# Performance work log

Hardware: AMD Instinct MI355X
Metric: run time of the kernel (lower is better)

Reference implementation:

```python
import jax, jax.numpy as jnp
import numpy as np
import math

B, S, H, NH = 2, 2048, 1024, 16
DK = H // NH


def setup_inputs() -> dict:
    key = jax.random.key(0)
    ks = jax.random.split(key, 12)
    s = 1.0 / math.sqrt(H)
    return {
        "query": jax.random.normal(ks[0], (B, S, H), jnp.float32),
        "key": jax.random.normal(ks[1], (B, S, H), jnp.float32),
        "value": jax.random.normal(ks[2], (B, S, H), jnp.float32),
        "attention_mask": jax.random.randint(ks[3], (B, S), 0, 2, jnp.int32),
        "Wq": jax.random.normal(ks[4], (H, H), jnp.float32) * s,
        "bq": jnp.zeros((H,), jnp.float32),
        "Wk": jax.random.normal(ks[5], (H, H), jnp.float32) * s,
        "bk": jnp.zeros((H,), jnp.float32),
        "Wv": jax.random.normal(ks[6], (H, H), jnp.float32) * s,
        "bv": jnp.zeros((H,), jnp.float32),
        "Wo": jax.random.normal(ks[7], (H, H), jnp.float32) * s,
        "bo": jnp.zeros((H,), jnp.float32),
    }


def reference(query, key, value, attention_mask, Wq, bq, Wk, bk, Wv, bv, Wo, bo):
    # linear projections (torch Linear: x @ W^T + b)
    q = query @ Wq.T + bq
    k = key @ Wk.T + bk
    v = value @ Wv.T + bv
    # [B, S, H] -> [B, NH, S, DK]
    q = q.reshape(B, S, NH, DK).transpose(0, 2, 1, 3)
    k = k.reshape(B, S, NH, DK).transpose(0, 2, 1, 3)
    v = v.reshape(B, S, NH, DK).transpose(0, 2, 1, 3)
    # scaled dot-product scores [B, NH, S, S]
    scores = jnp.einsum("bhqd,bhkd->bhqk", q, k) / math.sqrt(DK)
    # faithful to original: masked positions set to 1e-9 (NOT -inf)
    mask = attention_mask[:, None, None, :]  # [B,1,1,S]
    scores = jnp.where(mask == 0, jnp.float32(1e-9), scores)
    weights = jax.nn.softmax(scores, axis=-1)
    # dropout_prob = 0.0 (eval) -> identity
    context = jnp.einsum("bhqk,bhkd->bhqd", weights, v)
    context = context.transpose(0, 2, 1, 3).reshape(B, S, H)
    return context @ Wo.T + bo
```

## Files before the change

kernel.cpp:

```cpp
#include <hip/hip_runtime.h>
#include <stdint.h>

#define B_ 2
#define S_ 2048
#define H_ 1024
#define NH_ 16
#define DK_ 64
#define M_ (B_*S_)

typedef __attribute__((ext_vector_type(8))) short short8;
typedef __attribute__((ext_vector_type(4))) float f32x4;
typedef __attribute__((ext_vector_type(16))) float f32x16;
typedef __attribute__((ext_vector_type(4))) unsigned u32x4;

#define GLDS16(g, s) __builtin_amdgcn_global_load_lds( \
    (const __attribute__((address_space(1))) unsigned int*)(g), \
    (__attribute__((address_space(3))) unsigned int*)(s), 16, 0, 0)

__device__ __forceinline__ unsigned short f2bf(float x) {
  union { float f; unsigned u; } c; c.f = x;
  unsigned r = (c.u + 0x7FFF + ((c.u >> 16) & 1)) >> 16;
  return (unsigned short)r;
}

__global__ void k_cvt3(const float4* __restrict__ a, const float4* __restrict__ b,
                       const float4* __restrict__ c,
                       ushort4* __restrict__ oa, ushort4* __restrict__ ob,
                       ushort4* __restrict__ oc) {
  int idx = blockIdx.x * 256 + threadIdx.x;
  int t = idx >> 20, i = idx & ((1 << 20) - 1);
  const float4* s = (t == 0) ? a : (t == 1) ? b : c;
  ushort4* o = (t == 0) ? oa : (t == 1) ? ob : oc;
  float4 v = s[i];
  ushort4 r; r.x = f2bf(v.x); r.y = f2bf(v.y); r.z = f2bf(v.z); r.w = f2bf(v.w);
  o[i] = r;
}

__global__ void k_cvtw(const float4* __restrict__ a, const float4* __restrict__ b,
                       const float4* __restrict__ c, const float4* __restrict__ d,
                       ushort4* __restrict__ oa, ushort4* __restrict__ ob,
                       ushort4* __restrict__ oc, ushort4* __restrict__ od) {
  int idx = blockIdx.x * 256 + threadIdx.x;
  int t = idx >> 18, i = idx & ((1 << 18) - 1);
  const float4* s = (t == 0) ? a : (t == 1) ? b : (t == 2) ? c : d;
  ushort4* o = (t == 0) ? oa : (t == 1) ? ob : (t == 2) ? oc : od;
  float4 v = s[i];
  ushort4 r; r.x = f2bf(v.x); r.y = f2bf(v.y); r.z = f2bf(v.z); r.w = f2bf(v.w);
  o[i] = r;
}

enum { MODE_Q = 0, MODE_K = 1, MODE_VT = 2, MODE_F32 = 3 };

__device__ __forceinline__ void gemm_body(
    const unsigned short* __restrict__ A, const unsigned short* __restrict__ Bw,
    const float* __restrict__ bias, const int* __restrict__ amask,
    void* __restrict__ Cout, int mode, int bx, int by) {
  __shared__ unsigned short As[128 * 64];
  __shared__ unsigned short Bs[128 * 64];
  const int tid = threadIdx.x;
  const int w = tid >> 6, lane = tid & 63;
  const int lr = lane & 15, hi = lane >> 4;
  const int wr = w >> 1, wc = w & 1;
  const int m0 = by * 128, n0 = bx * 128;

  f32x4 acc[4][4];
#pragma unroll
  for (int i = 0; i < 4; i++)
#pragma unroll
    for (int j = 0; j < 4; j++) acc[i][j] = (f32x4){0.f, 0.f, 0.f, 0.f};

  for (int k0 = 0; k0 < H_; k0 += 64) {
    __syncthreads();
#pragma unroll
    for (int it = 0; it < 4; ++it) {
      int c = it * 256 + tid;
      int row = c >> 3, ch = c & 7;
      const unsigned short* ga = A + (size_t)(m0 + row) * H_ + k0 + ((ch ^ (row & 7)) << 3);
      GLDS16(ga, As + (it * 256 + w * 64) * 8);
      const unsigned short* gb = Bw + (size_t)(n0 + row) * H_ + k0 + ((ch ^ (row & 7)) << 3);
      GLDS16(gb, Bs + (it * 256 + w * 64) * 8);
    }
    __syncthreads();
#pragma unroll
    for (int ks = 0; ks < 2; ++ks) {
      short8 af[4], bfg[4];
#pragma unroll
      for (int mi = 0; mi < 4; ++mi) {
        int row = wr * 64 + mi * 16 + lr;
        int ch = ((ks << 2) | hi) ^ (lr & 7);
        af[mi] = *(const short8*)((const char*)As + row * 128 + (ch << 4));
      }
#pragma unroll
      for (int ni = 0; ni < 4; ++ni) {
        int row = wc * 64 + ni * 16 + lr;
        int ch = ((ks << 2) | hi) ^ (lr & 7);
        bfg[ni] = *(const short8*)((const char*)Bs + row * 128 + (ch << 4));
      }
#pragma unroll
      for (int mi = 0; mi < 4; ++mi)
#pragma unroll
        for (int ni = 0; ni < 4; ++ni)
          acc[mi][ni] = __builtin_amdgcn_mfma_f32_16x16x32_bf16(af[mi], bfg[ni], acc[mi][ni], 0, 0, 0);
    }
  }

  float bvv[4];
#pragma unroll
  for (int ni = 0; ni < 4; ++ni) bvv[ni] = bias[n0 + wc * 64 + ni * 16 + lr];

  if (mode == MODE_Q || mode == MODE_K) {
    unsigned short* C = (unsigned short*)Cout;
    float km[4][4];
    if (mode == MODE_K) {
#pragma unroll
      for (int mi = 0; mi < 4; ++mi)
#pragma unroll
        for (int j = 0; j < 4; ++j) {
          int r = m0 + wr * 64 + mi * 16 + hi * 4 + j;
          km[mi][j] = amask[r] ? 1.0f : 0.0f;
        }
    }
#pragma unroll
    for (int mi = 0; mi < 4; ++mi)
#pragma unroll
      for (int ni = 0; ni < 4; ++ni) {
        int col = n0 + wc * 64 + ni * 16 + lr;
#pragma unroll
        for (int j = 0; j < 4; ++j) {
          int r = m0 + wr * 64 + mi * 16 + hi * 4 + j;
          float v = acc[mi][ni][j] + bvv[ni];
          v *= (mode == MODE_Q) ? 0.125f : km[mi][j];
          C[(size_t)r * H_ + col] = f2bf(v);
        }
      }
  } else if (mode == MODE_F32) {
    float* C = (float*)Cout;
#pragma unroll
    for (int mi = 0; mi < 4; ++mi)
#pragma unroll
      for (int ni = 0; ni < 4; ++ni) {
        int col = n0 + wc * 64 + ni * 16 + lr;
#pragma unroll
        for (int j = 0; j < 4; ++j) {
          int r = m0 + wr * 64 + mi * 16 + hi * 4 + j;
          C[(size_t)r * H_ + col] = acc[mi][ni][j] + bvv[ni];
        }
      }
  } else {
    unsigned short* Vt = (unsigned short*)Cout;
#pragma unroll
    for (int mi = 0; mi < 4; ++mi) {
      int rbase = m0 + wr * 64 + mi * 16 + hi * 4;
      int bb = rbase >> 11, s0 = rbase & (S_ - 1);
#pragma unroll
      for (int ni = 0; ni < 4; ++ni) {
        int col = n0 + wc * 64 + ni * 16 + lr;
        ushort4 pk;
        pk.x = f2bf(acc[mi][ni][0] + bvv[ni]);
        pk.y = f2bf(acc[mi][ni][1] + bvv[ni]);
        pk.z = f2bf(acc[mi][ni][2] + bvv[ni]);
        pk.w = f2bf(acc[mi][ni][3] + bvv[ni]);
        *(ushort4*)(Vt + (size_t)(bb * H_ + col) * S_ + s0) = pk;
      }
    }
  }
}

__global__ __launch_bounds__(256, 2) void k_gemm_qkv(
    const unsigned short* __restrict__ Xq, const unsigned short* __restrict__ Xk,
    const unsigned short* __restrict__ Xv,
    const unsigned short* __restrict__ Wqb, const unsigned short* __restrict__ Wkb,
    const unsigned short* __restrict__ Wvb,
    const float* __restrict__ bq, const float* __restrict__ bk,
    const float* __restrict__ bv, const int* __restrict__ amask,
    unsigned short* __restrict__ Qb, unsigned short* __restrict__ Kb,
    unsigned short* __restrict__ Vtb) {
  int z = blockIdx.z;
  const unsigned short* A = (z == 0) ? Xq : (z == 1) ? Xk : Xv;
  const unsigned short* W = (z == 0) ? Wqb : (z == 1) ? Wkb : Wvb;
  const float* bias = (z == 0) ? bq : (z == 1) ? bk : bv;
  void* C = (z == 0) ? (void*)Qb : (z == 1) ? (void*)Kb : (void*)Vtb;
  int mode = (z == 0) ? MODE_Q : (z == 1) ? MODE_K : MODE_VT;
  gemm_body(A, W, bias, amask, C, mode, blockIdx.x, blockIdx.y);
}

__global__ __launch_bounds__(256, 2) void k_gemm_o(
    const unsigned short* __restrict__ Ctx, const unsigned short* __restrict__ Wob,
    const float* __restrict__ bo, float* __restrict__ out) {
  gemm_body(Ctx, Wob, bo, nullptr, (void*)out, MODE_F32, blockIdx.x, blockIdx.y);
}

__global__ __launch_bounds__(256, 2) void k_attn(
    const unsigned short* __restrict__ Qb, const unsigned short* __restrict__ Kb,
    const unsigned short* __restrict__ Vtb, unsigned short* __restrict__ Ctx) {
  __shared__ unsigned short Klds[64 * 64];
  __shared__ unsigned short Vtl[64 * 64];

  const int tid = threadIdx.x;
  const int w = tid >> 6, lane = tid & 63;
  const int l5 = lane & 31, hi5 = lane >> 5;
  int bid = (blockIdx.x & 7) * 64 + (blockIdx.x >> 3);
  const int qt = bid & 15;
  const int h = (bid >> 4) & 15;
  const int b = bid >> 8;
  const int qr = qt * 128 + w * 32 + l5;

  short8 aq[4];
  {
    const unsigned short* qp = Qb + (size_t)(b * S_ + qr) * H_ + h * DK_ + hi5 * 8;
#pragma unroll
    for (int dkblk = 0; dkblk < 4; ++dkblk)
      aq[dkblk] = *(const short8*)(qp + dkblk * 16);
  }

  const unsigned short* ksrc[2];
  const unsigned short* vsrc[2];
#pragma unroll
  for (int it = 0; it < 2; ++it) {
    int c = it * 256 + tid;
    int rho = c >> 3, cl = c & 7;
    int kap = 32 * (rho >> 5) + ((rho & 19) | ((rho & 4) << 1) | ((rho & 8) >> 1));
    ksrc[it] = Kb + (size_t)(b * S_ + kap) * H_ + h * DK_ + ((cl ^ (rho & 7)) << 3);
    vsrc[it] = Vtb + (size_t)(b * H_ + h * DK_ + rho) * S_ + ((cl ^ (rho & 7)) << 3);
  }

  f32x16 ctx[2];
#pragma unroll
  for (int dblk = 0; dblk < 2; ++dblk)
#pragma unroll
    for (int i = 0; i < 16; ++i) ctx[dblk][i] = 0.f;
  float mrun = -30000.f, lrun = 0.f;

  for (int kv0 = 0; kv0 < S_; kv0 += 64) {
    __syncthreads();
#pragma unroll
    for (int it = 0; it < 2; ++it) {
      GLDS16(ksrc[it] + (size_t)kv0 * H_, Klds + (it * 256 + w * 64) * 8);
      GLDS16(vsrc[it] + kv0, Vtl + (it * 256 + w * 64) * 8);
    }
    __syncthreads();

    f32x16 sc[2];
#pragma unroll
    for (int kb = 0; kb < 2; ++kb) {
      f32x16 a;
#pragma unroll
      for (int i = 0; i < 16; ++i) a[i] = 0.f;
#pragma unroll
      for (int dkblk = 0; dkblk < 4; ++dkblk) {
        int row = kb * 32 + l5;
        int ch = (2 * dkblk + hi5) ^ (row & 7);
        short8 kf = *(const short8*)((const char*)Klds + row * 128 + (ch << 4));
        a = __builtin_amdgcn_mfma_f32_32x32x16_bf16(kf, aq[dkblk], a, 0, 0, 0);
      }
      sc[kb] = a;
    }

    float mx = sc[0][0];
#pragma unroll
    for (int i = 1; i < 16; ++i) mx = fmaxf(mx, sc[0][i]);
#pragma unroll
    for (int i = 0; i < 16; ++i) mx = fmaxf(mx, sc[1][i]);
    mx = fmaxf(mx, __shfl_xor(mx, 32));
    float mnew = fmaxf(mrun, mx);
    float scale = __expf(mrun - mnew);
    float ps = 0.f;
#pragma unroll
    for (int kb = 0; kb < 2; ++kb)
#pragma unroll
      for (int i = 0; i < 16; ++i) {
        float e = __expf(sc[kb][i] - mnew);
        sc[kb][i] = e;
        ps += e;
      }
    ps += __shfl_xor(ps, 32);
    lrun = lrun * scale + ps;
    mrun = mnew;
#pragma unroll
    for (int dblk = 0; dblk < 2; ++dblk)
#pragma unroll
      for (int i = 0; i < 16; ++i) ctx[dblk][i] *= scale;

#pragma unroll
    for (int kb = 0; kb < 2; ++kb)
#pragma unroll
      for (int u = 0; u < 2; ++u) {
        unsigned w0, w1, w2, w3;
        asm("v_cvt_pk_bf16_f32 %0, %1, %2" : "=v"(w0) : "v"(sc[kb][8*u+0]), "v"(sc[kb][8*u+1]));
        asm("v_cvt_pk_bf16_f32 %0, %1, %2" : "=v"(w1) : "v"(sc[kb][8*u+2]), "v"(sc[kb][8*u+3]));
        asm("v_cvt_pk_bf16_f32 %0, %1, %2" : "=v"(w2) : "v"(sc[kb][8*u+4]), "v"(sc[kb][8*u+5]));
        asm("v_cvt_pk_bf16_f32 %0, %1, %2" : "=v"(w3) : "v"(sc[kb][8*u+6]), "v"(sc[kb][8*u+7]));
        u32x4 wp; wp.x = w0; wp.y = w1; wp.z = w2; wp.w = w3;
        short8 pb = __builtin_bit_cast(short8, wp);
#pragma unroll
        for (int dblk = 0; dblk < 2; ++dblk) {
          int row = dblk * 32 + l5;
          int ch = (4 * kb + 2 * u + hi5) ^ (row & 7);
          short8 vt = *(const short8*)((const char*)Vtl + row * 128 + (ch << 4));
          ctx[dblk] = __builtin_amdgcn_mfma_f32_32x32x16_bf16(vt, pb, ctx[dblk], 0, 0, 0);
        }
      }
  }

  float inv = 1.0f / lrun;
  unsigned short* cp = Ctx + (size_t)(b * S_ + qr) * H_ + h * DK_;
#pragma unroll
  for (int dblk = 0; dblk < 2; ++dblk)
#pragma unroll
    for (int s = 0; s < 4; ++s) {
      ushort4 o;
      o.x = f2bf(ctx[dblk][4*s+0] * inv);
      o.y = f2bf(ctx[dblk][4*s+1] * inv);
      o.z = f2bf(ctx[dblk][4*s+2] * inv);
      o.w = f2bf(ctx[dblk][4*s+3] * inv);
      *(ushort4*)(cp + dblk * 32 + 8 * s + 4 * hi5) = o;
    }
}

extern "C" void kernel_launch(void* const* d_in, const int* in_sizes, int n_in,
                              void* d_out, int out_size, void* d_ws, size_t ws_size,
                              hipStream_t stream) {
  (void)in_sizes; (void)n_in; (void)out_size; (void)ws_size;
  const float* query = (const float*)d_in[0];
  const float* key   = (const float*)d_in[1];
  const float* value = (const float*)d_in[2];
  const int*   amask = (const int*)d_in[3];
  const float* Wq = (const float*)d_in[4];
  const float* bq = (const float*)d_in[5];
  const float* Wk = (const float*)d_in[6];
  const float* bk = (const float*)d_in[7];
  const float* Wv = (const float*)d_in[8];
  const float* bv = (const float*)d_in[9];
  const float* Wo = (const float*)d_in[10];
  const float* bo = (const float*)d_in[11];
  float* out = (float*)d_out;

  unsigned short* ws = (unsigned short*)d_ws;
  const size_t SZX = (size_t)M_ * H_;
  const size_t SZW = (size_t)H_ * H_;
  unsigned short* Xq  = ws;
  unsigned short* Xk  = Xq + SZX;
  unsigned short* Xv  = Xk + SZX;
  unsigned short* Wqb = Xv + SZX;
  unsigned short* Wkb = Wqb + SZW;
  unsigned short* Wvb = Wkb + SZW;
  unsigned short* Wob = Wvb + SZW;
  unsigned short* Qb  = Wob + SZW;
  unsigned short* Kb  = Qb + SZX;
  unsigned short* Vtb = Kb + SZX;
  unsigned short* Ctx = Vtb + SZX;

  k_cvt3<<<dim3(12288), dim3(256), 0, stream>>>(
      (const float4*)query, (const float4*)key, (const float4*)value,
      (ushort4*)Xq, (ushort4*)Xk, (ushort4*)Xv);
  k_cvtw<<<dim3(4096), dim3(256), 0, stream>>>(
      (const float4*)Wq, (const float4*)Wk, (const float4*)Wv, (const float4*)Wo,
      (ushort4*)Wqb, (ushort4*)Wkb, (ushort4*)Wvb, (ushort4*)Wob);
  k_gemm_qkv<<<dim3(8, 32, 3), dim3(256), 0, stream>>>(
      Xq, Xk, Xv, Wqb, Wkb, Wvb, bq, bk, bv, amask, Qb, Kb, Vtb);
  k_attn<<<dim3(512), dim3(256), 0, stream>>>(Qb, Kb, Vtb, Ctx);
  k_gemm_o<<<dim3(8, 32), dim3(256), 0, stream>>>(Ctx, Wob, bo, out);
}
```

Measured before the change: 227.6 us.

## Double-buffer LDS in GEMM and attention, shrink attention blocks, add exp2 lazy rescale

Both the projection GEMM and the attention kernel now keep two LDS buffers, issuing the global-to-LDS loads for the next K tile before computing on the current one. This halves the barriers per iteration and hides load latency. The attention kernel moves to 128-thread blocks covering 64 query rows each, on a grid twice as large. Q is pre-scaled by log2(e)/8 so the softmax can use exp2, and the running-max rescale of the accumulators is skipped unless the max grows by more than 8. This trades doubled LDS per block and some numerical headroom for better overlap and fewer exponentials.

Measured after the change: 270.6 us. 18.9% more time.

```diff
diff --git a/kernel.cpp b/kernel.cpp
--- a/kernel.cpp
+++ b/kernel.cpp
@@ -55,32 +55,46 @@
     const unsigned short* __restrict__ A, const unsigned short* __restrict__ Bw,
     const float* __restrict__ bias, const int* __restrict__ amask,
     void* __restrict__ Cout, int mode, int bx, int by) {
-  __shared__ unsigned short As[128 * 64];
-  __shared__ unsigned short Bs[128 * 64];
+  __shared__ unsigned short As[2][128 * 64];
+  __shared__ unsigned short Bs[2][128 * 64];
   const int tid = threadIdx.x;
   const int w = tid >> 6, lane = tid & 63;
   const int lr = lane & 15, hi = lane >> 4;
   const int wr = w >> 1, wc = w & 1;
   const int m0 = by * 128, n0 = bx * 128;
 
+  const unsigned short* asrc[4];
+  const unsigned short* bsrc[4];
+#pragma unroll
+  for (int it = 0; it < 4; ++it) {
+    int c = it * 256 + tid;
+    int row = c >> 3, ch = c & 7;
+    asrc[it] = A + (size_t)(m0 + row) * H_ + ((ch ^ (row & 7)) << 3);
+    bsrc[it] = Bw + (size_t)(n0 + row) * H_ + ((ch ^ (row & 7)) << 3);
+  }
+
   f32x4 acc[4][4];
 #pragma unroll
   for (int i = 0; i < 4; i++)
 #pragma unroll
     for (int j = 0; j < 4; j++) acc[i][j] = (f32x4){0.f, 0.f, 0.f, 0.f};
 
+#pragma unroll
+  for (int it = 0; it < 4; ++it) {
+    GLDS16(asrc[it], &As[0][(it * 256 + w * 64) * 8]);
+    GLDS16(bsrc[it], &Bs[0][(it * 256 + w * 64) * 8]);
+  }
+  __syncthreads();
+
   for (int k0 = 0; k0 < H_; k0 += 64) {
-    __syncthreads();
-#pragma unroll
-    for (int it = 0; it < 4; ++it) {
-      int c = it * 256 + tid;
-      int row = c >> 3, ch = c & 7;
-      const unsigned short* ga = A + (size_t)(m0 + row) * H_ + k0 + ((ch ^ (row & 7)) << 3);
-      GLDS16(ga, As + (it * 256 + w * 64) * 8);
-      const unsigned short* gb = Bw + (size_t)(n0 + row) * H_ + k0 + ((ch ^ (row & 7)) << 3);
-      GLDS16(gb, Bs + (it * 256 + w * 64) * 8);
-    }
-    __syncthreads();
+    const int cur = (k0 >> 6) & 1;
+    if (k0 + 64 < H_) {
+#pragma unroll
+      for (int it = 0; it < 4; ++it) {
+        GLDS16(asrc[it] + k0 + 64, &As[cur ^ 1][(it * 256 + w * 64) * 8]);
+        GLDS16(bsrc[it] + k0 + 64, &Bs[cur ^ 1][(it * 256 + w * 64) * 8]);
+      }
+    }
 #pragma unroll
     for (int ks = 0; ks < 2; ++ks) {
       short8 af[4], bfg[4];
@@ -88,13 +102,13 @@
       for (int mi = 0; mi < 4; ++mi) {
         int row = wr * 64 + mi * 16 + lr;
         int ch = ((ks << 2) | hi) ^ (lr & 7);
-        af[mi] = *(const short8*)((const char*)As + row * 128 + (ch << 4));
+        af[mi] = *(const short8*)((const char*)As[cur] + row * 128 + (ch << 4));
       }
 #pragma unroll
       for (int ni = 0; ni < 4; ++ni) {
         int row = wc * 64 + ni * 16 + lr;
         int ch = ((ks << 2) | hi) ^ (lr & 7);
-        bfg[ni] = *(const short8*)((const char*)Bs + row * 128 + (ch << 4));
+        bfg[ni] = *(const short8*)((const char*)Bs[cur] + row * 128 + (ch << 4));
       }
 #pragma unroll
       for (int mi = 0; mi < 4; ++mi)
@@ -102,6 +116,7 @@
         for (int ni = 0; ni < 4; ++ni)
           acc[mi][ni] = __builtin_amdgcn_mfma_f32_16x16x32_bf16(af[mi], bfg[ni], acc[mi][ni], 0, 0, 0);
     }
+    __syncthreads();
   }
 
   float bvv[4];
@@ -129,7 +144,7 @@
         for (int j = 0; j < 4; ++j) {
           int r = m0 + wr * 64 + mi * 16 + hi * 4 + j;
           float v = acc[mi][ni][j] + bvv[ni];
-          v *= (mode == MODE_Q) ? 0.125f : km[mi][j];
+          v *= (mode == MODE_Q) ? 0.180336879f : km[mi][j];
           C[(size_t)r * H_ + col] = f2bf(v);
         }
       }
@@ -190,20 +205,20 @@
   gemm_body(Ctx, Wob, bo, nullptr, (void*)out, MODE_F32, blockIdx.x, blockIdx.y);
 }
 
-__global__ __launch_bounds__(256, 2) void k_attn(
+__global__ __launch_bounds__(128, 2) void k_attn(
     const unsigned short* __restrict__ Qb, const unsigned short* __restrict__ Kb,
     const unsigned short* __restrict__ Vtb, unsigned short* __restrict__ Ctx) {
-  __shared__ unsigned short Klds[64 * 64];
-  __shared__ unsigned short Vtl[64 * 64];
+  __shared__ unsigned short Klds[2][64 * 64];
+  __shared__ unsigned short Vtl[2][64 * 64];
 
   const int tid = threadIdx.x;
   const int w = tid >> 6, lane = tid & 63;
   const int l5 = lane & 31, hi5 = lane >> 5;
-  int bid = (blockIdx.x & 7) * 64 + (blockIdx.x >> 3);
-  const int qt = bid & 15;
-  const int h = (bid >> 4) & 15;
-  const int b = bid >> 8;
-  const int qr = qt * 128 + w * 32 + l5;
+  int bid = (blockIdx.x & 7) * 128 + (blockIdx.x >> 3);
+  const int qt = bid & 31;
+  const int h = (bid >> 5) & 15;
+  const int b = bid >> 9;
+  const int qr = qt * 64 + w * 32 + l5;
 
   short8 aq[4];
   {
@@ -213,11 +228,11 @@
       aq[dkblk] = *(const short8*)(qp + dkblk * 16);
   }
 
-  const unsigned short* ksrc[2];
-  const unsigned short* vsrc[2];
-#pragma unroll
-  for (int it = 0; it < 2; ++it) {
-    int c = it * 256 + tid;
+  const unsigned short* ksrc[4];
+  const unsigned short* vsrc[4];
+#pragma unroll
+  for (int it = 0; it < 4; ++it) {
+    int c = it * 128 + tid;
     int rho = c >> 3, cl = c & 7;
     int kap = 32 * (rho >> 5) + ((rho & 19) | ((rho & 4) << 1) | ((rho & 8) >> 1));
     ksrc[it] = Kb + (size_t)(b * S_ + kap) * H_ + h * DK_ + ((cl ^ (rho & 7)) << 3);
@@ -231,14 +246,23 @@
     for (int i = 0; i < 16; ++i) ctx[dblk][i] = 0.f;
   float mrun = -30000.f, lrun = 0.f;
 
-  for (int kv0 = 0; kv0 < S_; kv0 += 64) {
-    __syncthreads();
-#pragma unroll
-    for (int it = 0; it < 2; ++it) {
-      GLDS16(ksrc[it] + (size_t)kv0 * H_, Klds + (it * 256 + w * 64) * 8);
-      GLDS16(vsrc[it] + kv0, Vtl + (it * 256 + w * 64) * 8);
-    }
-    __syncthreads();
+#pragma unroll
+  for (int it = 0; it < 4; ++it) {
+    GLDS16(ksrc[it], &Klds[0][(it * 128 + w * 64) * 8]);
+    GLDS16(vsrc[it], &Vtl[0][(it * 128 + w * 64) * 8]);
+  }
+  __syncthreads();
+
+  for (int t = 0; t < S_ / 64; ++t) {
+    const int cur = t & 1;
+    if (t + 1 < S_ / 64) {
+      int kv1 = (t + 1) * 64;
+#pragma unroll
+      for (int it = 0; it < 4; ++it) {
+        GLDS16(ksrc[it] + (size_t)kv1 * H_, &Klds[cur ^ 1][(it * 128 + w * 64) * 8]);
+        GLDS16(vsrc[it] + kv1, &Vtl[cur ^ 1][(it * 128 + w * 64) * 8]);
+      }
+    }
 
     f32x16 sc[2];
 #pragma unroll
@@ -250,7 +274,7 @@
       for (int dkblk = 0; dkblk < 4; ++dkblk) {
         int row = kb * 32 + l5;
         int ch = (2 * dkblk + hi5) ^ (row & 7);
-        short8 kf = *(const short8*)((const char*)Klds + row * 128 + (ch << 4));
+        short8 kf = *(const short8*)((const char*)Klds[cur] + row * 128 + (ch << 4));
         a = __builtin_amdgcn_mfma_f32_32x32x16_bf16(kf, aq[dkblk], a, 0, 0, 0);
       }
       sc[kb] = a;
@@ -262,24 +286,27 @@
 #pragma unroll
     for (int i = 0; i < 16; ++i) mx = fmaxf(mx, sc[1][i]);
     mx = fmaxf(mx, __shfl_xor(mx, 32));
-    float mnew = fmaxf(mrun, mx);
-    float scale = __expf(mrun - mnew);
+    if (!__all(mx <= mrun + 8.f)) {
+      float mnew = fmaxf(mrun, mx);
+      float scale = exp2f(mrun - mnew);
+      mrun = mnew;
+      lrun *= scale;
+#pragma unroll
+      for (int dblk = 0; dblk < 2; ++dblk)
+#pragma unroll
+        for (int i = 0; i < 16; ++i) ctx[dblk][i] *= scale;
+    }
     float ps = 0.f;
 #pragma unroll
     for (int kb = 0; kb < 2; ++kb)
 #pragma unroll
       for (int i = 0; i < 16; ++i) {
-        float e = __expf(sc[kb][i] - mnew);
+        float e = exp2f(sc[kb][i] - mrun);
         sc[kb][i] = e;
         ps += e;
       }
     ps += __shfl_xor(ps, 32);
-    lrun = lrun * scale + ps;
-    mrun = mnew;
-#pragma unroll
-    for (int dblk = 0; dblk < 2; ++dblk)
-#pragma unroll
-      for (int i = 0; i < 16; ++i) ctx[dblk][i] *= scale;
+    lrun += ps;
 
 #pragma unroll
     for (int kb = 0; kb < 2; ++kb)
@@ -296,10 +323,12 @@
         for (int dblk = 0; dblk < 2; ++dblk) {
           int row = dblk * 32 + l5;
           int ch = (4 * kb + 2 * u + hi5) ^ (row & 7);
-          short8 vt = *(const short8*)((const char*)Vtl + row * 128 + (ch << 4));
+          short8 vt = *(const short8*)((const char*)Vtl[cur] + row * 128 + (ch << 4));
           ctx[dblk] = __builtin_amdgcn_mfma_f32_32x32x16_bf16(vt, pb, ctx[dblk], 0, 0, 0);
         }
       }
+
+    __syncthreads();
   }
 
   float inv = 1.0f / lrun;
@@ -358,6 +387,6 @@
       (ushort4*)Wqb, (ushort4*)Wkb, (ushort4*)Wvb, (ushort4*)Wob);
   k_gemm_qkv<<<dim3(8, 32, 3), dim3(256), 0, stream>>>(
       Xq, Xk, Xv, Wqb, Wkb, Wvb, bq, bk, bv, amask, Qb, Kb, Vtb);
-  k_attn<<<dim3(512), dim3(256), 0, stream>>>(Qb, Kb, Vtb, Ctx);
+  k_attn<<<dim3(1024), dim3(128), 0, stream>>>(Qb, Kb, Vtb, Ctx);
   k_gemm_o<<<dim3(8, 32), dim3(256), 0, stream>>>(Ctx, Wob, bo, out);
 }
```
